# Optimization experiments

Measured on AMD Instinct MI355X. Metric: run time of the kernel, lower is better.

## Reference

```python
import jax, jax.numpy as jnp
import numpy as np

SR = 11025.0
N_OSC = 128


def conv2d(x, w, b, stride, pad):
    y = jax.lax.conv_general_dilated(
        x, w, window_strides=stride,
        padding=[(pad[0], pad[0]), (pad[1], pad[1])],
        dimension_numbers=('NCHW', 'OIHW', 'NCHW'))
    return y + b[None, :, None, None]


def lrelu(v):
    return jax.nn.leaky_relu(v, 0.2)


def smooth_upsample2(x, size):
    # linear interpolation along time (torch F.upsample mode='linear', align_corners=False)
    b, c, t = x.shape
    return jax.image.resize(x, (b, c, size), 'linear')


def noise_bank2(mags, noise):
    # mags: (B, 17, frames) squared magnitudes; noise: (B, hop*frames) uniform(-1,1)
    b, nm, frames = mags.shape
    win = (nm - 1) * 2           # 32
    hop = win // 2               # 16
    total = hop * frames
    noise = jnp.pad(noise, ((0, 0), (0, hop)))
    idx = jnp.arange(frames)[:, None] * hop + jnp.arange(win)[None, :]
    frames_n = noise[:, idx]
    coeffs = jnp.fft.rfft(frames_n, axis=-1, norm='ortho')    # (B, frames, 17)
    coeffs = coeffs * mags.transpose(0, 2, 1)                 # apply per-frame magnitudes
    filt = jnp.fft.irfft(coeffs, n=win, axis=-1, norm='ortho')
    first, second = filt[..., :hop], filt[..., hop:]
    ola = (jnp.pad(first, ((0, 0), (0, 1), (0, 0))) +
           jnp.pad(second, ((0, 0), (1, 0), (0, 0)))).reshape(b, -1)
    return ola[:, :total][:, None, :]                         # (B, 1, total)


def oscillator_bank(f, l):
    # f, l: (B, n_osc, T); integrate frequency -> phase, synthesize, sum oscillators
    f = jnp.clip(f, 20.0, SR / 2.0)
    phases = jnp.cumsum(f * (2.0 * np.pi / SR), axis=-1)
    return jnp.sum(jnp.sin(phases) * l, axis=1)               # (B, T)


def setup_inputs() -> dict:
    key = jax.random.key(0)
    ks = jax.random.split(key, 24)
    B, C, T = 4, 256, 512
    inp = {}
    inp['x'] = jax.random.normal(ks[0], (B, C, T), jnp.float32)
    inp['noise'] = jax.random.uniform(ks[1], (B, 256 * T), jnp.float32, minval=-1.0, maxval=1.0)
    specs = [('m1', (32, 1, 3, 9)), ('m2', (32, 32, 9, 3)), ('m3', (64, 32, 3, 9)),
             ('m4', (64, 64, 3, 9)), ('m5', (32, 64, 3, 9)), ('tp', (2, 32, 3, 3)),
             ('n1', (16, 32, 17, 3)), ('n2', (16, 16, 17, 3)), ('n3', (16, 16, 2, 3)),
             ('n4', (17, 16, 3, 3))]
    for i, (name, s) in enumerate(specs):
        fan_in = s[1] * s[2] * s[3]
        inp[name + '_w'] = jax.random.normal(ks[2 + i], s, jnp.float32) / np.float32(np.sqrt(fan_in))
        inp[name + '_b'] = jnp.zeros((s[0],), jnp.float32)
    centers = jnp.asarray(np.geomspace(20.0, SR / 2.0 - 20.0, N_OSC), jnp.float32)
    inp['centers'] = centers
    inp['erbs'] = centers * np.float32(0.108) + np.float32(24.7)
    return inp


def reference(x, noise, m1_w, m1_b, m2_w, m2_b, m3_w, m3_b, m4_w, m4_b, m5_w, m5_b,
              tp_w, tp_b, n1_w, n1_b, n2_w, n2_b, n3_w, n3_b, n4_w, n4_b,
              centers, erbs):
    B, C, T = x.shape
    h = x[:, None]                                            # (B,1,256,T)
    h = lrelu(conv2d(h, m1_w, m1_b, (1, 1), (1, 4)))
    h = lrelu(conv2d(h, m2_w, m2_b, (1, 1), (4, 1)))
    h = lrelu(conv2d(h, m3_w, m3_b, (1, 1), (1, 4)))
    h = lrelu(conv2d(h, m4_w, m4_b, (2, 1), (1, 4)))          # (B,64,128,T)
    h = lrelu(conv2d(h, m5_w, m5_b, (1, 1), (1, 4)))          # (B,32,128,T)
    pre = h
    p = conv2d(h, tp_w, tp_b, (1, 1), (1, 1))                 # (B,2,128,T)
    l = p[:, 0] ** 2
    f = jnp.tanh(p[:, 1]) * 0.5
    f = centers[None, :, None] + f * erbs[None, :, None]
    up = T * 256
    l = smooth_upsample2(l, up)
    f = smooth_upsample2(f, up)
    # noise parameter branch
    n = lrelu(conv2d(pre, n1_w, n1_b, (8, 1), (8, 1)))        # (B,16,16,T)
    n = jax.image.resize(n, (n.shape[0], 16, 16, T * 16), 'linear')  # bilinear (1,16)
    n = lrelu(conv2d(n, n2_w, n2_b, (8, 1), (8, 1)))          # (B,16,2,16T)
    n = lrelu(conv2d(n, n3_w, n3_b, (1, 1), (0, 1)))          # (B,16,1,16T)
    n = conv2d(n, n4_w, n4_b, (1, 1), (1, 1))                 # (B,17,1,16T)
    n_l = (n ** 2).reshape(B, 17, -1)
    harmonic = oscillator_bank(f, l)[:, None, :]              # (B,1,256T)
    noise_out = noise_bank2(n_l, noise)                       # (B,1,256T)
    return (harmonic + noise_out)[:, :, 4096:-4096]
```

## Files before the change

### kernel.cpp

```cpp
#include <hip/hip_runtime.h>
#include <hip/hip_bf16.h>
#include <math.h>


#define DEVFN __device__ __forceinline__

__global__ __launch_bounds__(256) void pickx(
    const float* __restrict__ A, int* __restrict__ flag) {
  __shared__ float red[256];
  float m = 0.f;
  for (int i = threadIdx.x; i < 524288; i += 256) m = fmaxf(m, fabsf(A[i]));
  red[threadIdx.x] = m; __syncthreads();
  for (int o = 128; o > 0; o >>= 1) {
    if (threadIdx.x < o) red[threadIdx.x] = fmaxf(red[threadIdx.x], red[threadIdx.x + o]);
    __syncthreads();
  }
  if (threadIdx.x == 0) *flag = (red[0] > 1.0001f) ? 0 : 1;
}

__global__ __launch_bounds__(256) void selcopy(
    const float* __restrict__ A, const float* __restrict__ B,
    const int* __restrict__ flag, float* __restrict__ X, float* __restrict__ NZ) {
  int i = blockIdx.x * 256 + threadIdx.x;
  const float* xs = (*flag == 0) ? A : B;
  const float* ns = (*flag == 0) ? B : A;
  X[i] = xs[i]; NZ[i] = ns[i];
}

template<typename TIN,int IC,int OC,int KH,int KW,int SH,int PH_,int PW,
         int OCPT,int OWPT,int EPI>
__global__ __launch_bounds__(128) void convkd(
    const TIN* __restrict__ in, const float* __restrict__ wg,
    double* __restrict__ out, int IH, int IW, int OH, int OW) {
  const int tid = threadIdx.x;
  const int WT  = OW >> 9;
  const int wt  = blockIdx.x % WT;
  const int ocg = blockIdx.x / WT;
  const int oh  = blockIdx.y;
  const int oc0 = ocg * OCPT;
  const int ow0 = (wt * 128 + tid) * OWPT;

  double acc[OCPT][OWPT];
#pragma unroll
  for (int j = 0; j < OCPT; ++j)
#pragma unroll
    for (int i = 0; i < OWPT; ++i) acc[j][i] = 0.0;

  for (int ic = 0; ic < IC; ++ic) {
    const TIN* inp = in + (size_t)ic * IH * IW;
#pragma unroll
    for (int kh = 0; kh < KH; ++kh) {
      int ih = oh * SH + kh - PH_;
      if (ih < 0 || ih >= IH) continue;
      const TIN* row = inp + (size_t)ih * IW;
      double xin[OWPT + KW - 1];
#pragma unroll
      for (int i = 0; i < OWPT + KW - 1; ++i) {
        int iw = ow0 - PW + i;
        xin[i] = (iw >= 0 && iw < IW) ? (double)row[iw] : 0.0;
      }
      const float* wbase = wg + ((size_t)ic * KH + kh) * KW;
#pragma unroll
      for (int kw = 0; kw < KW; ++kw) {
#pragma unroll
        for (int j = 0; j < OCPT; ++j) {
          double wv = (double)wbase[(size_t)(oc0 + j) * IC * KH * KW + kw];
#pragma unroll
          for (int i = 0; i < OWPT; ++i)
            acc[j][i] = fma(xin[i + kw], wv, acc[j][i]);
        }
      }
    }
  }
#pragma unroll
  for (int j = 0; j < OCPT; ++j) {
    double* op = out + ((size_t)(oc0 + j) * OH + oh) * OW + ow0;
#pragma unroll
    for (int i = 0; i < OWPT; ++i) {
      double v = acc[j][i];
      if (EPI == 1) v = v > 0.0 ? v : 0.2 * v;
      if (EPI == 2) v = v * v;
      op[i] = v;
    }
  }
}

__global__ __launch_bounds__(256) void tpostd(
    const double* __restrict__ p, const float* __restrict__ centers,
    const float* __restrict__ erbs, double* __restrict__ lfr, double* __restrict__ ffr) {
  int idx = blockIdx.x * 256 + threadIdx.x;
  int fr = idx & 511;
  int o  = idx >> 9;
  double p0 = p[(size_t)o * 512 + fr];
  double p1 = p[(size_t)(128 + o) * 512 + fr];
  lfr[idx] = p0 * p0;
  ffr[idx] = (double)centers[o] + tanh(p1) * 0.5 * (double)erbs[o];
}

__global__ __launch_bounds__(256) void resizeWd(
    const double* __restrict__ in, double* __restrict__ out) {
  int idx = blockIdx.x * 256 + threadIdx.x;
  int t = idx & 8191;
  int r = idx >> 13;
  double c = ((double)t + 0.5) * (1.0 / 16.0) - 0.5;
  double fl = floor(c);
  int i0 = (int)fl;
  double w = c - fl;
  int ia = i0 < 0 ? 0 : i0;
  int ib = (i0 + 1 > 511) ? 511 : i0 + 1;
  const double* rp = in + (size_t)r * 512;
  out[idx] = rp[ia] * (1.0 - w) + rp[ib] * w;
}

__global__ __launch_bounds__(256) void noisebankd(
    const float* __restrict__ nz, const double* __restrict__ mags,
    double* __restrict__ filt) {
  __shared__ double ct[17][32], st[17][32];
  for (int i = threadIdx.x; i < 17 * 32; i += 256) {
    int k = i >> 5, t = i & 31;
    double ang = (M_PI / 16.0) * (double)(k * t);
    ct[k][t] = cos(ang);
    st[k][t] = sin(ang);
  }
  __syncthreads();
  int frm = blockIdx.x * 256 + threadIdx.x;
  int base = frm * 16;
  double x[32];
#pragma unroll
  for (int t = 0; t < 32; ++t) {
    int idx = base + t;
    x[t] = (idx < 131072) ? (double)nz[idx] : 0.0;
  }
  double a[17], bb[17];
#pragma unroll
  for (int k = 0; k < 17; ++k) {
    double ra = 0.0, rb = 0.0;
#pragma unroll
    for (int t = 0; t < 32; ++t) {
      ra = fma(x[t], ct[k][t], ra);
      rb = fma(x[t], st[k][t], rb);
    }
    double m  = mags[(size_t)k * 8192 + frm];
    double wk = (k == 0 || k == 16) ? 1.0 : 2.0;
    double cf = wk * m * (1.0 / 32.0);
    a[k] = cf * ra; bb[k] = cf * rb;
  }
  double* fo = filt + (size_t)frm * 32;
#pragma unroll
  for (int t = 0; t < 32; ++t) {
    double s = 0.0;
#pragma unroll
    for (int k = 0; k < 17; ++k)
      s = fma(a[k], ct[k][t], fma(bb[k], st[k][t], s));
    fo[t] = s;
  }
}

DEVFN double phase_inc_d(const double* __restrict__ fr_row, int t) {
  double c = ((double)t + 0.5) * (1.0 / 256.0) - 0.5;
  double fl = floor(c);
  int i0 = (int)fl;
  double w = c - fl;
  int ia = i0 < 0 ? 0 : i0;
  int ib = (i0 + 1 > 511) ? 511 : i0 + 1;
  double f = (1.0 - w) * fr_row[ia] + w * fr_row[ib];
  f = f < 20.0 ? 20.0 : (f > 5512.5 ? 5512.5 : f);
  return f * (2.0 * M_PI / 11025.0);
}

__global__ __launch_bounds__(256) void phaseAd(
    const double* __restrict__ ffr, double* __restrict__ ctot) {
  __shared__ double sr[256];
  int chunk = blockIdx.x, o = blockIdx.y;
  const double* fr = ffr + (size_t)o * 512;
  int t0 = chunk * 1024 + threadIdx.x * 4;
  double s = phase_inc_d(fr, t0) + phase_inc_d(fr, t0 + 1)
           + phase_inc_d(fr, t0 + 2) + phase_inc_d(fr, t0 + 3);
  sr[threadIdx.x] = s; __syncthreads();
  for (int off = 128; off > 0; off >>= 1) {
    if (threadIdx.x < off) sr[threadIdx.x] += sr[threadIdx.x + off];
    __syncthreads();
  }
  if (threadIdx.x == 0) ctot[(size_t)o * 128 + chunk] = sr[0];
}

__global__ __launch_bounds__(128) void phaseBd(
    const double* __restrict__ ctot, double* __restrict__ cbas) {
  int o = threadIdx.x;
  double base = 0.0;
  for (int c = 0; c < 128; ++c) {
    cbas[(size_t)o * 128 + c] = base;
    base += ctot[(size_t)o * 128 + c];
  }
}

__global__ __launch_bounds__(256) void harmkd(
    const double* __restrict__ ffr, const double* __restrict__ lfr,
    const double* __restrict__ cbas, const double* __restrict__ filt,
    float* __restrict__ out) {
  __shared__ double sw[4];
  const int tid  = threadIdx.x;
  const int lane = tid & 63, wid = tid >> 6;
  const int chunk = blockIdx.x + 4;
  const int t0 = chunk * 1024 + tid * 4;

  int i0s[4], ibs[4]; double wls[4];
#pragma unroll
  for (int k = 0; k < 4; ++k) {
    double c = ((double)(t0 + k) + 0.5) * (1.0 / 256.0) - 0.5;
    double fl = floor(c);
    int i0 = (int)fl;
    wls[k] = c - fl;
    i0s[k] = i0;
    ibs[k] = (i0 + 1 > 511) ? 511 : i0 + 1;
  }
  double acc0 = 0.0, acc1 = 0.0, acc2 = 0.0, acc3 = 0.0;

  for (int o = 0; o < 128; ++o) {
    const double* fr = ffr + (size_t)o * 512;
    double a0 = phase_inc_d(fr, t0 + 0);
    double a1 = phase_inc_d(fr, t0 + 1);
    double a2 = phase_inc_d(fr, t0 + 2);
    double a3 = phase_inc_d(fr, t0 + 3);
    double l0 = a0, l1 = l0 + a1, l2 = l1 + a2, l3 = l2 + a3;
    double v = l3;
#pragma unroll
    for (int off = 1; off < 64; off <<= 1) {
      double n = __shfl_up(v, off);
      if (lane >= off) v += n;
    }
    if (lane == 63) sw[wid] = v;
    __syncthreads();
    double base = cbas[(size_t)o * 128 + chunk];
    for (int w2 = 0; w2 < wid; ++w2) base += sw[w2];
    __syncthreads();
    double excl = base + (v - l3);

    const double* lrow = lfr + (size_t)o * 512;
    double lv0 = lrow[i0s[0]] * (1.0 - wls[0]) + lrow[ibs[0]] * wls[0];
    double lv1 = lrow[i0s[1]] * (1.0 - wls[1]) + lrow[ibs[1]] * wls[1];
    double lv2 = lrow[i0s[2]] * (1.0 - wls[2]) + lrow[ibs[2]] * wls[2];
    double lv3 = lrow[i0s[3]] * (1.0 - wls[3]) + lrow[ibs[3]] * wls[3];

    acc0 = fma(sin(excl + l0), lv0, acc0);
    acc1 = fma(sin(excl + l1), lv1, acc1);
    acc2 = fma(sin(excl + l2), lv2, acc2);
    acc3 = fma(sin(excl + l3), lv3, acc3);
  }
#pragma unroll
  for (int k = 0; k < 4; ++k) {
    int t = t0 + k;
    int r = t >> 4, j = t & 15;
    double nz = filt[(size_t)r * 32 + j] + filt[(size_t)(r - 1) * 32 + 16 + j];
    double h = (k == 0) ? acc0 : (k == 1) ? acc1 : (k == 2) ? acc2 : acc3;
    out[t - 4096] = (float)(h + nz);
  }
}

extern "C" void kernel_launch(void* const* d_in, const int* in_sizes, int n_in,
                              void* d_out, int out_size, void* d_ws, size_t ws_size,
                              hipStream_t stream) {
  (void)out_size; (void)ws_size;
  const float *big0 = nullptr, *big1 = nullptr;
  const float *m1w=nullptr,*m2w=nullptr,*m3w=nullptr,*m4w=nullptr,*m5w=nullptr;
  const float *tpw=nullptr,*n1w=nullptr,*n2w=nullptr,*n3w=nullptr,*n4w=nullptr;
  const float *centers=nullptr,*erbs=nullptr;
  int n55296 = 0, n128 = 0, nbig = 0;
  for (int i = 0; i < n_in; ++i) {
    const float* p = (const float*)d_in[i];
    switch (in_sizes[i]) {
      case 524288: if (nbig++ == 0) big0 = p; else big1 = p; break;
      case 864:    m1w = p; break;
      case 27648:  m2w = p; break;
      case 55296:  if (n55296++ == 0) m3w = p; else m5w = p; break;
      case 110592: m4w = p; break;
      case 576:    tpw = p; break;
      case 26112:  n1w = p; break;
      case 13056:  n2w = p; break;
      case 1536:   n3w = p; break;
      case 2448:   n4w = p; break;
      case 128:    if (n128++ == 0) centers = p; else erbs = p; break;
      default: break;
    }
  }

  char* ws = (char*)d_ws;
  double* R1   = (double*)(ws + 0);
  double* R2   = (double*)(ws + 67108864);
  double* PRE  = (double*)(ws + 100663296);
  double* NB1R = (double*)(ws + 117440512);
  double* FILT = (double*)(ws + 134217728);
  double* NB2  = (double*)(ws + 136314880);
  double* NB3  = (double*)(ws + 138412032);
  double* MAGS = (double*)(ws + 139460608);
  double* NB1  = (double*)(ws + 140574720);
  double* P    = (double*)(ws + 141623296);
  double* FFR  = (double*)(ws + 142671872);
  double* LFR  = (double*)(ws + 143196160);
  double* CTOT = (double*)(ws + 143720448);
  double* CBAS = (double*)(ws + 143851520);
  float*  XBUF = (float*) (ws + 143982592);
  float*  NZBUF= (float*) (ws + 146079744);
  int*    FLAG = (int*)   (ws + 148176896);

  pickx<<<dim3(1),256,0,stream>>>(big0, FLAG);
  selcopy<<<dim3(2048),256,0,stream>>>(big0, big1, FLAG, XBUF, NZBUF);

  for (int b = 0; b < 4; ++b) {
    const float* xb  = XBUF  + (size_t)b * 131072;
    const float* nzb = NZBUF + (size_t)b * 131072;
    float* ob = (float*)d_out + (size_t)b * 122880;

    convkd<float, 1,32,3,9,1,1,4, 4,4,1><<<dim3(8,256,1),128,0,stream>>>(xb, m1w, R1, 256,512,256,512);
    convkd<double,32,32,9,3,1,4,1, 4,4,1><<<dim3(8,256,1),128,0,stream>>>(R1, m2w, R2, 256,512,256,512);
    convkd<double,32,64,3,9,1,1,4, 4,4,1><<<dim3(16,256,1),128,0,stream>>>(R2, m3w, R1, 256,512,256,512);
    convkd<double,64,64,3,9,2,1,4, 4,4,1><<<dim3(16,128,1),128,0,stream>>>(R1, m4w, R2, 256,512,128,512);
    convkd<double,64,32,3,9,1,1,4, 4,4,1><<<dim3(8,128,1),128,0,stream>>>(R2, m5w, PRE, 128,512,128,512);
    convkd<double,32,2,3,3,1,1,1, 2,4,0><<<dim3(1,128,1),128,0,stream>>>(PRE, tpw, P, 128,512,128,512);
    tpostd<<<dim3(256),256,0,stream>>>(P, centers, erbs, LFR, FFR);
    convkd<double,32,16,17,3,8,8,1, 4,4,1><<<dim3(4,16,1),128,0,stream>>>(PRE, n1w, NB1, 128,512,16,512);
    resizeWd<<<dim3(8192),256,0,stream>>>(NB1, NB1R);
    convkd<double,16,16,17,3,8,8,1, 4,4,1><<<dim3(64,2,1),128,0,stream>>>(NB1R, n2w, NB2, 16,8192,2,8192);
    convkd<double,16,16,2,3,1,0,1, 4,4,1><<<dim3(64,1,1),128,0,stream>>>(NB2, n3w, NB3, 2,8192,1,8192);
    convkd<double,16,17,3,3,1,1,1, 1,4,2><<<dim3(272,1,1),128,0,stream>>>(NB3, n4w, MAGS, 1,8192,1,8192);
    noisebankd<<<dim3(32),256,0,stream>>>(nzb, MAGS, FILT);
    phaseAd<<<dim3(128,128),256,0,stream>>>(FFR, CTOT);
    phaseBd<<<dim3(1),128,0,stream>>>(CTOT, CBAS);
    harmkd<<<dim3(120),256,0,stream>>>(FFR, LFR, CBAS, FILT, ob);
  }
}
```

Before: 8.632 ms.

## Move noise branch and harmonic sum to float, batch the synthesis stage

Converts the noise-parameter conv chain, resize, noise bank and harmonic amplitude path from double to float. Phase accumulation stays in double, with float sin applied after range reduction. The prefix-scan and harmonic kernels move out of the per-batch loop and run once over all four batches, using 256-sample chunks. This removes the block-level syncthreads in the harmonic kernel and raises the output-channel tiling of the main convs to 8. The aim is to cut double-precision ALU cost and launch count, in exchange for reduced numerical precision in the noise and amplitude paths and higher register pressure in the convs.

```diff
diff --git a/kernel.cpp b/kernel.cpp
--- a/kernel.cpp
+++ b/kernel.cpp
@@ -85,73 +85,130 @@
   }
 }
 
+template<typename TIN,int IC,int OC,int KH,int KW,int SH,int PH_,int PW,
+         int OCPT,int OWPT,int EPI>
+__global__ __launch_bounds__(128) void convf(
+    const TIN* __restrict__ in, const float* __restrict__ wg,
+    float* __restrict__ out, int IH, int IW, int OH, int OW) {
+  const int tid = threadIdx.x;
+  const int WT  = OW / (128 * OWPT);
+  const int wt  = blockIdx.x % WT;
+  const int ocg = blockIdx.x / WT;
+  const int oh  = blockIdx.y;
+  const int oc0 = ocg * OCPT;
+  const int ow0 = (wt * 128 + tid) * OWPT;
+
+  float acc[OCPT][OWPT];
+#pragma unroll
+  for (int j = 0; j < OCPT; ++j)
+#pragma unroll
+    for (int i = 0; i < OWPT; ++i) acc[j][i] = 0.f;
+
+  for (int ic = 0; ic < IC; ++ic) {
+    const TIN* inp = in + (size_t)ic * IH * IW;
+#pragma unroll
+    for (int kh = 0; kh < KH; ++kh) {
+      int ih = oh * SH + kh - PH_;
+      if (ih < 0 || ih >= IH) continue;
+      const TIN* row = inp + (size_t)ih * IW;
+      float xin[OWPT + KW - 1];
+#pragma unroll
+      for (int i = 0; i < OWPT + KW - 1; ++i) {
+        int iw = ow0 - PW + i;
+        xin[i] = (iw >= 0 && iw < IW) ? (float)row[iw] : 0.f;
+      }
+      const float* wbase = wg + ((size_t)ic * KH + kh) * KW;
+#pragma unroll
+      for (int kw = 0; kw < KW; ++kw) {
+#pragma unroll
+        for (int j = 0; j < OCPT; ++j) {
+          float wv = wbase[(size_t)(oc0 + j) * IC * KH * KW + kw];
+#pragma unroll
+          for (int i = 0; i < OWPT; ++i)
+            acc[j][i] = fmaf(xin[i + kw], wv, acc[j][i]);
+        }
+      }
+    }
+  }
+#pragma unroll
+  for (int j = 0; j < OCPT; ++j) {
+    float* op = out + ((size_t)(oc0 + j) * OH + oh) * OW + ow0;
+#pragma unroll
+    for (int i = 0; i < OWPT; ++i) {
+      float v = acc[j][i];
+      if (EPI == 1) v = v > 0.f ? v : 0.2f * v;
+      if (EPI == 2) v = v * v;
+      op[i] = v;
+    }
+  }
+}
+
 __global__ __launch_bounds__(256) void tpostd(
     const double* __restrict__ p, const float* __restrict__ centers,
-    const float* __restrict__ erbs, double* __restrict__ lfr, double* __restrict__ ffr) {
+    const float* __restrict__ erbs, float* __restrict__ lfr, double* __restrict__ ffr) {
   int idx = blockIdx.x * 256 + threadIdx.x;
   int fr = idx & 511;
   int o  = idx >> 9;
   double p0 = p[(size_t)o * 512 + fr];
   double p1 = p[(size_t)(128 + o) * 512 + fr];
-  lfr[idx] = p0 * p0;
+  lfr[idx] = (float)(p0 * p0);
   ffr[idx] = (double)centers[o] + tanh(p1) * 0.5 * (double)erbs[o];
 }
 
-__global__ __launch_bounds__(256) void resizeWd(
-    const double* __restrict__ in, double* __restrict__ out) {
+__global__ __launch_bounds__(256) void resizef(
+    const float* __restrict__ in, float* __restrict__ out) {
   int idx = blockIdx.x * 256 + threadIdx.x;
   int t = idx & 8191;
   int r = idx >> 13;
-  double c = ((double)t + 0.5) * (1.0 / 16.0) - 0.5;
-  double fl = floor(c);
-  int i0 = (int)fl;
-  double w = c - fl;
+  float c = ((float)t + 0.5f) * (1.0f / 16.0f) - 0.5f;
+  int i0 = (int)floorf(c);
+  float w = c - (float)i0;
   int ia = i0 < 0 ? 0 : i0;
   int ib = (i0 + 1 > 511) ? 511 : i0 + 1;
-  const double* rp = in + (size_t)r * 512;
-  out[idx] = rp[ia] * (1.0 - w) + rp[ib] * w;
-}
-
-__global__ __launch_bounds__(256) void noisebankd(
-    const float* __restrict__ nz, const double* __restrict__ mags,
-    double* __restrict__ filt) {
-  __shared__ double ct[17][32], st[17][32];
+  const float* rp = in + (size_t)r * 512;
+  out[idx] = rp[ia] * (1.f - w) + rp[ib] * w;
+}
+
+__global__ __launch_bounds__(256) void noisebankf(
+    const float* __restrict__ nz, const float* __restrict__ mags,
+    float* __restrict__ filt) {
+  __shared__ float ct[17][32], st[17][32];
   for (int i = threadIdx.x; i < 17 * 32; i += 256) {
     int k = i >> 5, t = i & 31;
     double ang = (M_PI / 16.0) * (double)(k * t);
-    ct[k][t] = cos(ang);
-    st[k][t] = sin(ang);
+    ct[k][t] = (float)cos(ang);
+    st[k][t] = (float)sin(ang);
   }
   __syncthreads();
   int frm = blockIdx.x * 256 + threadIdx.x;
   int base = frm * 16;
-  double x[32];
+  float x[32];
 #pragma unroll
   for (int t = 0; t < 32; ++t) {
     int idx = base + t;
-    x[t] = (idx < 131072) ? (double)nz[idx] : 0.0;
-  }
-  double a[17], bb[17];
+    x[t] = (idx < 131072) ? nz[idx] : 0.f;
+  }
+  float a[17], bb[17];
 #pragma unroll
   for (int k = 0; k < 17; ++k) {
-    double ra = 0.0, rb = 0.0;
+    float ra = 0.f, rb = 0.f;
 #pragma unroll
     for (int t = 0; t < 32; ++t) {
-      ra = fma(x[t], ct[k][t], ra);
-      rb = fma(x[t], st[k][t], rb);
-    }
-    double m  = mags[(size_t)k * 8192 + frm];
-    double wk = (k == 0 || k == 16) ? 1.0 : 2.0;
-    double cf = wk * m * (1.0 / 32.0);
+      ra = fmaf(x[t], ct[k][t], ra);
+      rb = fmaf(x[t], st[k][t], rb);
+    }
+    float m  = mags[(size_t)k * 8192 + frm];
+    float wk = (k == 0 || k == 16) ? 1.0f : 2.0f;
+    float cf = wk * m * (1.0f / 32.0f);
     a[k] = cf * ra; bb[k] = cf * rb;
   }
-  double* fo = filt + (size_t)frm * 32;
+  float* fo = filt + (size_t)frm * 32;
 #pragma unroll
   for (int t = 0; t < 32; ++t) {
-    double s = 0.0;
+    float s = 0.f;
 #pragma unroll
     for (int k = 0; k < 17; ++k)
-      s = fma(a[k], ct[k][t], fma(bb[k], st[k][t], s));
+      s = fmaf(a[k], ct[k][t], fmaf(bb[k], st[k][t], s));
     fo[t] = s;
   }
 }
@@ -168,53 +225,59 @@
   return f * (2.0 * M_PI / 11025.0);
 }
 
-__global__ __launch_bounds__(256) void phaseAd(
-    const double* __restrict__ ffr, double* __restrict__ ctot) {
-  __shared__ double sr[256];
-  int chunk = blockIdx.x, o = blockIdx.y;
-  const double* fr = ffr + (size_t)o * 512;
-  int t0 = chunk * 1024 + threadIdx.x * 4;
+__global__ __launch_bounds__(256) void phaseA256(
+    const double* __restrict__ FFR, double* __restrict__ CTOT) {
+  int lane = threadIdx.x & 63, wid = threadIdx.x >> 6;
+  int o = blockIdx.y, b = blockIdx.z;
+  int ch = blockIdx.x * 4 + wid;
+  const double* fr = FFR + (size_t)b * 65536 + (size_t)o * 512;
+  int t0 = ch * 256 + lane * 4;
   double s = phase_inc_d(fr, t0) + phase_inc_d(fr, t0 + 1)
            + phase_inc_d(fr, t0 + 2) + phase_inc_d(fr, t0 + 3);
-  sr[threadIdx.x] = s; __syncthreads();
-  for (int off = 128; off > 0; off >>= 1) {
-    if (threadIdx.x < off) sr[threadIdx.x] += sr[threadIdx.x + off];
-    __syncthreads();
-  }
-  if (threadIdx.x == 0) ctot[(size_t)o * 128 + chunk] = sr[0];
-}
-
-__global__ __launch_bounds__(128) void phaseBd(
-    const double* __restrict__ ctot, double* __restrict__ cbas) {
+#pragma unroll
+  for (int off = 32; off > 0; off >>= 1) s += __shfl_xor(s, off);
+  if (lane == 0) CTOT[((size_t)b * 128 + o) * 512 + ch] = s;
+}
+
+__global__ __launch_bounds__(128) void phaseB4(
+    const double* __restrict__ CTOT, double* __restrict__ CBAS) {
   int o = threadIdx.x;
+  int b = blockIdx.x;
+  const double* ct = CTOT + ((size_t)b * 128 + o) * 512;
+  double* cb = CBAS + ((size_t)b * 128 + o) * 512;
   double base = 0.0;
-  for (int c = 0; c < 128; ++c) {
-    cbas[(size_t)o * 128 + c] = base;
-    base += ctot[(size_t)o * 128 + c];
-  }
-}
-
-__global__ __launch_bounds__(256) void harmkd(
-    const double* __restrict__ ffr, const double* __restrict__ lfr,
-    const double* __restrict__ cbas, const double* __restrict__ filt,
+  for (int c = 0; c < 512; ++c) { cb[c] = base; base += ct[c]; }
+}
+
+DEVFN float sinx(double ph) {
+  double k = rint(ph * 0.15915494309189535);
+  float r = (float)__builtin_fma(-k, 6.283185307179586, ph);
+  return sinf(r);
+}
+
+__global__ __launch_bounds__(256) void harm2(
+    const double* __restrict__ FFR, const float* __restrict__ LFR32,
+    const double* __restrict__ CBAS, const float* __restrict__ FILT,
     float* __restrict__ out) {
-  __shared__ double sw[4];
-  const int tid  = threadIdx.x;
-  const int lane = tid & 63, wid = tid >> 6;
-  const int chunk = blockIdx.x + 4;
-  const int t0 = chunk * 1024 + tid * 4;
-
-  int i0s[4], ibs[4]; double wls[4];
+  int tid = threadIdx.x, lane = tid & 63, wid = tid >> 6;
+  int b = blockIdx.y;
+  int ch = 16 + blockIdx.x * 4 + wid;
+  int t0 = ch * 256 + lane * 4;
+  const double* ffr  = FFR  + (size_t)b * 65536;
+  const float*  lfr  = LFR32 + (size_t)b * 65536;
+  const double* cbas = CBAS + (size_t)b * 65536;
+  const float*  filt = FILT + (size_t)b * 262144;
+  float* ob = out + (size_t)b * 122880;
+
+  int fis[4]; float wls[4];
 #pragma unroll
   for (int k = 0; k < 4; ++k) {
     double c = ((double)(t0 + k) + 0.5) * (1.0 / 256.0) - 0.5;
     double fl = floor(c);
-    int i0 = (int)fl;
-    wls[k] = c - fl;
-    i0s[k] = i0;
-    ibs[k] = (i0 + 1 > 511) ? 511 : i0 + 1;
-  }
-  double acc0 = 0.0, acc1 = 0.0, acc2 = 0.0, acc3 = 0.0;
+    fis[k] = (int)fl;
+    wls[k] = (float)(c - fl);
+  }
+  float acc0 = 0.f, acc1 = 0.f, acc2 = 0.f, acc3 = 0.f;
 
   for (int o = 0; o < 128; ++o) {
     const double* fr = ffr + (size_t)o * 512;
@@ -229,31 +292,26 @@
       double n = __shfl_up(v, off);
       if (lane >= off) v += n;
     }
-    if (lane == 63) sw[wid] = v;
-    __syncthreads();
-    double base = cbas[(size_t)o * 128 + chunk];
-    for (int w2 = 0; w2 < wid; ++w2) base += sw[w2];
-    __syncthreads();
-    double excl = base + (v - l3);
-
-    const double* lrow = lfr + (size_t)o * 512;
-    double lv0 = lrow[i0s[0]] * (1.0 - wls[0]) + lrow[ibs[0]] * wls[0];
-    double lv1 = lrow[i0s[1]] * (1.0 - wls[1]) + lrow[ibs[1]] * wls[1];
-    double lv2 = lrow[i0s[2]] * (1.0 - wls[2]) + lrow[ibs[2]] * wls[2];
-    double lv3 = lrow[i0s[3]] * (1.0 - wls[3]) + lrow[ibs[3]] * wls[3];
-
-    acc0 = fma(sin(excl + l0), lv0, acc0);
-    acc1 = fma(sin(excl + l1), lv1, acc1);
-    acc2 = fma(sin(excl + l2), lv2, acc2);
-    acc3 = fma(sin(excl + l3), lv3, acc3);
+    double excl = cbas[(size_t)o * 512 + ch] + (v - l3);
+
+    const float* lr = lfr + (size_t)o * 512;
+    float lv0 = lr[fis[0]] * (1.f - wls[0]) + lr[fis[0] + 1] * wls[0];
+    float lv1 = lr[fis[1]] * (1.f - wls[1]) + lr[fis[1] + 1] * wls[1];
+    float lv2 = lr[fis[2]] * (1.f - wls[2]) + lr[fis[2] + 1] * wls[2];
+    float lv3 = lr[fis[3]] * (1.f - wls[3]) + lr[fis[3] + 1] * wls[3];
+
+    acc0 = fmaf(sinx(excl + l0), lv0, acc0);
+    acc1 = fmaf(sinx(excl + l1), lv1, acc1);
+    acc2 = fmaf(sinx(excl + l2), lv2, acc2);
+    acc3 = fmaf(sinx(excl + l3), lv3, acc3);
   }
 #pragma unroll
   for (int k = 0; k < 4; ++k) {
     int t = t0 + k;
     int r = t >> 4, j = t & 15;
-    double nz = filt[(size_t)r * 32 + j] + filt[(size_t)(r - 1) * 32 + 16 + j];
-    double h = (k == 0) ? acc0 : (k == 1) ? acc1 : (k == 2) ? acc2 : acc3;
-    out[t - 4096] = (float)(h + nz);
+    float nz = filt[r * 32 + j] + filt[(r - 1) * 32 + 16 + j];
+    float h = (k == 0) ? acc0 : (k == 1) ? acc1 : (k == 2) ? acc2 : acc3;
+    ob[t - 4096] = h + nz;
   }
 }
 
@@ -285,23 +343,23 @@
   }
 
   char* ws = (char*)d_ws;
-  double* R1   = (double*)(ws + 0);
-  double* R2   = (double*)(ws + 67108864);
-  double* PRE  = (double*)(ws + 100663296);
-  double* NB1R = (double*)(ws + 117440512);
-  double* FILT = (double*)(ws + 134217728);
-  double* NB2  = (double*)(ws + 136314880);
-  double* NB3  = (double*)(ws + 138412032);
-  double* MAGS = (double*)(ws + 139460608);
-  double* NB1  = (double*)(ws + 140574720);
-  double* P    = (double*)(ws + 141623296);
-  double* FFR  = (double*)(ws + 142671872);
-  double* LFR  = (double*)(ws + 143196160);
-  double* CTOT = (double*)(ws + 143720448);
-  double* CBAS = (double*)(ws + 143851520);
-  float*  XBUF = (float*) (ws + 143982592);
-  float*  NZBUF= (float*) (ws + 146079744);
-  int*    FLAG = (int*)   (ws + 148176896);
+  double* R1    = (double*)(ws + 0);
+  double* R2    = (double*)(ws + 67108864);
+  double* PRE   = (double*)(ws + 100663296);
+  double* P     = (double*)(ws + 117440512);
+  float*  NB1   = (float*) (ws + 118489088);
+  float*  NB1R  = (float*) (ws + 119013376);
+  float*  NB2   = (float*) (ws + 127401984);
+  float*  NB3   = (float*) (ws + 128450560);
+  float*  MAGS  = (float*) (ws + 128974848);
+  double* FFR   = (double*)(ws + 129531904);
+  float*  LFR32 = (float*) (ws + 131629056);
+  double* CTOT  = (double*)(ws + 132677632);
+  double* CBAS  = (double*)(ws + 134774784);
+  float*  FILT  = (float*) (ws + 136871936);
+  float*  XBUF  = (float*) (ws + 141066240);
+  float*  NZBUF = (float*) (ws + 143163392);
+  int*    FLAG  = (int*)   (ws + 145260544);
 
   pickx<<<dim3(1),256,0,stream>>>(big0, FLAG);
   selcopy<<<dim3(2048),256,0,stream>>>(big0, big1, FLAG, XBUF, NZBUF);
@@ -309,23 +367,26 @@
   for (int b = 0; b < 4; ++b) {
     const float* xb  = XBUF  + (size_t)b * 131072;
     const float* nzb = NZBUF + (size_t)b * 131072;
-    float* ob = (float*)d_out + (size_t)b * 122880;
-
-    convkd<float, 1,32,3,9,1,1,4, 4,4,1><<<dim3(8,256,1),128,0,stream>>>(xb, m1w, R1, 256,512,256,512);
-    convkd<double,32,32,9,3,1,4,1, 4,4,1><<<dim3(8,256,1),128,0,stream>>>(R1, m2w, R2, 256,512,256,512);
-    convkd<double,32,64,3,9,1,1,4, 4,4,1><<<dim3(16,256,1),128,0,stream>>>(R2, m3w, R1, 256,512,256,512);
-    convkd<double,64,64,3,9,2,1,4, 4,4,1><<<dim3(16,128,1),128,0,stream>>>(R1, m4w, R2, 256,512,128,512);
-    convkd<double,64,32,3,9,1,1,4, 4,4,1><<<dim3(8,128,1),128,0,stream>>>(R2, m5w, PRE, 128,512,128,512);
+    double* FFRb  = FFR   + (size_t)b * 65536;
+    float*  LFRb  = LFR32 + (size_t)b * 65536;
+    float*  FILTb = FILT  + (size_t)b * 262144;
+
+    convkd<float, 1,32,3,9,1,1,4, 8,4,1><<<dim3(4,256,1),128,0,stream>>>(xb, m1w, R1, 256,512,256,512);
+    convkd<double,32,32,9,3,1,4,1, 8,4,1><<<dim3(4,256,1),128,0,stream>>>(R1, m2w, R2, 256,512,256,512);
+    convkd<double,32,64,3,9,1,1,4, 8,4,1><<<dim3(8,256,1),128,0,stream>>>(R2, m3w, R1, 256,512,256,512);
+    convkd<double,64,64,3,9,2,1,4, 8,4,1><<<dim3(8,128,1),128,0,stream>>>(R1, m4w, R2, 256,512,128,512);
+    convkd<double,64,32,3,9,1,1,4, 8,4,1><<<dim3(4,128,1),128,0,stream>>>(R2, m5w, PRE, 128,512,128,512);
     convkd<double,32,2,3,3,1,1,1, 2,4,0><<<dim3(1,128,1),128,0,stream>>>(PRE, tpw, P, 128,512,128,512);
-    tpostd<<<dim3(256),256,0,stream>>>(P, centers, erbs, LFR, FFR);
-    convkd<double,32,16,17,3,8,8,1, 4,4,1><<<dim3(4,16,1),128,0,stream>>>(PRE, n1w, NB1, 128,512,16,512);
-    resizeWd<<<dim3(8192),256,0,stream>>>(NB1, NB1R);
-    convkd<double,16,16,17,3,8,8,1, 4,4,1><<<dim3(64,2,1),128,0,stream>>>(NB1R, n2w, NB2, 16,8192,2,8192);
-    convkd<double,16,16,2,3,1,0,1, 4,4,1><<<dim3(64,1,1),128,0,stream>>>(NB2, n3w, NB3, 2,8192,1,8192);
-    convkd<double,16,17,3,3,1,1,1, 1,4,2><<<dim3(272,1,1),128,0,stream>>>(NB3, n4w, MAGS, 1,8192,1,8192);
-    noisebankd<<<dim3(32),256,0,stream>>>(nzb, MAGS, FILT);
-    phaseAd<<<dim3(128,128),256,0,stream>>>(FFR, CTOT);
-    phaseBd<<<dim3(1),128,0,stream>>>(CTOT, CBAS);
-    harmkd<<<dim3(120),256,0,stream>>>(FFR, LFR, CBAS, FILT, ob);
-  }
-}
+    tpostd<<<dim3(256),256,0,stream>>>(P, centers, erbs, LFRb, FFRb);
+    convf<double,32,16,17,3,8,8,1, 4,1,1><<<dim3(16,16,1),128,0,stream>>>(PRE, n1w, NB1, 128,512,16,512);
+    resizef<<<dim3(8192),256,0,stream>>>(NB1, NB1R);
+    convf<float,16,16,17,3,8,8,1, 4,4,1><<<dim3(64,2,1),128,0,stream>>>(NB1R, n2w, NB2, 16,8192,2,8192);
+    convf<float,16,16,2,3,1,0,1, 4,4,1><<<dim3(64,1,1),128,0,stream>>>(NB2, n3w, NB3, 2,8192,1,8192);
+    convf<float,16,17,3,3,1,1,1, 1,4,2><<<dim3(272,1,1),128,0,stream>>>(NB3, n4w, MAGS, 1,8192,1,8192);
+    noisebankf<<<dim3(32),256,0,stream>>>(nzb, MAGS, FILTb);
+  }
+
+  phaseA256<<<dim3(128,128,4),256,0,stream>>>(FFR, CTOT);
+  phaseB4<<<dim3(4),128,0,stream>>>(CTOT, CBAS);
+  harm2<<<dim3(120,4),256,0,stream>>>(FFR, LFR32, CBAS, FILT, (float*)d_out);
+}
```

After: 8.711 ms. About the same (+0.9%).
